# Kernel tuning notes

Measured on AMD Instinct MI355X. Metric: run time of the kernel, lower is better.

The kernel has to match this reference:

```python
import jax, jax.numpy as jnp
import numpy as np

# Hardware / quantization constants (DacAdcHardwareSettings + quant scales)
INPUT_BITS = 8
OUT_PREC_BITS = 8          # fractional precision bits of the ADC
OUT_RANGE_BITS = 4         # ADC full-scale range = 2**OUT_RANGE_BITS
VMAX = 0.6                 # DAC output voltage full scale
OUT_SCALE = 8020.0         # hardware_output_current_scaling (current -> ADC units)
INPUT_FACTOR = 0.15        # 1/(activation scale * quant_max)
OUTPUT_FACTOR = 0.01       # weight scale * activation scale * quant_max
G_SCALE = 1e-4             # conductance magnitude (Siemens) for memristor cells
WEIGHT_PRECISION = 4       # -> 3 bit-plane memristor arrays


def dac(x):
    # clamp to [-1,1], quantize to INPUT_BITS signed levels, scale to volts
    levels = 2.0 ** (INPUT_BITS - 1) - 1.0
    return VMAX * jnp.round(jnp.clip(x, -1.0, 1.0) * levels) / levels


def adc(current):
    # scale current to ADC units, quantize with fixed fractional step, clip to range
    step = 2.0 ** (-OUT_PREC_BITS)
    rng = 2.0 ** OUT_RANGE_BITS
    scaled = current * OUT_SCALE
    return jnp.clip(jnp.round(scaled / step) * step, -rng, rng)


def setup_inputs() -> dict:
    key = jax.random.key(0)
    k0, k1, k2, k3 = jax.random.split(key, 4)
    tokens, d_in, d_out = 8192, 4096, 4096
    n_planes = WEIGHT_PRECISION - 1
    x = jax.random.normal(k0, (tokens, d_in), dtype=jnp.float32)
    # paired memristor conductances per bit plane, input-major [plane, in, out]
    w_pos = jax.random.uniform(k1, (n_planes, d_in, d_out), dtype=jnp.float32) * G_SCALE
    w_neg = jax.random.uniform(k2, (n_planes, d_in, d_out), dtype=jnp.float32) * G_SCALE
    bias = jax.random.normal(k3, (d_out,), dtype=jnp.float32)
    return {"x": x, "w_pos": w_pos, "w_neg": w_neg, "bias": bias}


def reference(x, w_pos, w_neg, bias):
    # DAC: quantize scaled activations to drive voltages
    inp = dac(x * INPUT_FACTOR)                      # [B, I]
    # effective bit-plane weights: positive minus negative cell conductances
    w_eff = w_pos - w_neg                            # [P, I, O]
    # crossbar readout for all bit planes: I = V @ G
    planes = jnp.einsum('bi,pio->pbo', inp, w_eff)   # [P, B, O]
    q = adc(planes)                                  # quantized per plane
    # shift-accumulate: memristors[-1] is bit 0; memristors[i] (i<P-2) is bit P-2-i
    p = w_eff.shape[0]
    shifts = jnp.array([2.0 ** (p - 1 - i) for i in range(p)],
                       dtype=x.dtype)
    shifts = shifts.at[-1].set(1.0)                  # [4., 2., 1.] for precision 4
    mem_out = jnp.einsum('pbo,p->bo', q, shifts)
    return mem_out * OUTPUT_FACTOR + bias
```

## Files before the change

### kernel.cpp

```cpp
#include <hip/hip_runtime.h>
#include <hip/hip_bf16.h>
#include <stdint.h>

#define TOK  8192
#define DIN  4096
#define DOUT 4096
#define NPL  3

typedef unsigned short u16;
typedef __attribute__((ext_vector_type(8))) __bf16 bf16x8;
typedef __attribute__((ext_vector_type(4))) float f32x4;
typedef __attribute__((ext_vector_type(4))) unsigned short u16x4;

#define ADC_MUL   9699.7795275590551f
#define INV256    0.00390625f

#define GL(src, dst) __builtin_amdgcn_global_load_lds( \
    (const __attribute__((address_space(1))) void*)(src), \
    (__attribute__((address_space(3))) void*)(dst), 16, 0, 0)

__global__ void dac_kernel(const float* __restrict__ x, u16* __restrict__ a) {
    const int n4 = TOK * DIN / 4;
    int i = blockIdx.x * blockDim.x + threadIdx.x;
    const int stride = gridDim.x * blockDim.x;
    const float4* xv = (const float4*)x;
    u16x4* av = (u16x4*)a;
    for (; i < n4; i += stride) {
        float4 v = xv[i];
        u16x4 o;
        float t, k;
        t = v.x * 0.15f; t = fminf(1.0f, fmaxf(-1.0f, t)); k = rintf(t * 127.0f);
        o.x = (u16)(__float_as_uint(k) >> 16);
        t = v.y * 0.15f; t = fminf(1.0f, fmaxf(-1.0f, t)); k = rintf(t * 127.0f);
        o.y = (u16)(__float_as_uint(k) >> 16);
        t = v.z * 0.15f; t = fminf(1.0f, fmaxf(-1.0f, t)); k = rintf(t * 127.0f);
        o.z = (u16)(__float_as_uint(k) >> 16);
        t = v.w * 0.15f; t = fminf(1.0f, fmaxf(-1.0f, t)); k = rintf(t * 127.0f);
        o.w = (u16)(__float_as_uint(k) >> 16);
        av[i] = o;
    }
}

__global__ void wsplit_kernel(const float* __restrict__ wp, const float* __restrict__ wn,
                              u16* __restrict__ w) {
    __shared__ float tile[64][65];
    const int b   = blockIdx.x;
    const int p   = b >> 12;
    const int rem = b & 4095;
    const int ib  = rem >> 6, ob = rem & 63;
    const int t   = threadIdx.x;
    const size_t plane = (size_t)p * DIN * DOUT;

    {
        const int o4 = (t & 15) << 2;
        const int r0 = t >> 4;
#pragma unroll
        for (int pass = 0; pass < 4; ++pass) {
            const int r = (pass << 4) + r0;
            const size_t off = plane + (size_t)(ib * 64 + r) * DOUT + ob * 64 + o4;
            const float4 a = *(const float4*)(wp + off);
            const float4 c = *(const float4*)(wn + off);
            tile[r][o4 + 0] = a.x - c.x;
            tile[r][o4 + 1] = a.y - c.y;
            tile[r][o4 + 2] = a.z - c.z;
            tile[r][o4 + 3] = a.w - c.w;
        }
    }
    __syncthreads();
    const int lane = t & 63, w4 = t >> 6;
#pragma unroll
    for (int pass = 0; pass < 16; ++pass) {
        const int o = (pass << 2) + w4;
        float d = tile[lane][o];
        uint32_t db = __float_as_uint(d);
        uint32_t hb = (db + 0x7fffu + ((db >> 16) & 1u)) & 0xffff0000u;
        float l = d - __uint_as_float(hb);
        uint32_t lb = __float_as_uint(l);
        u16 lo16 = (u16)((lb + 0x7fffu + ((lb >> 16) & 1u)) >> 16);
        size_t base = (size_t)(ob * 64 + o) * 24576 + (size_t)p * 8192 + ib * 128 + lane;
        w[base]      = (u16)(hb >> 16);
        w[base + 64] = lo16;
    }
}

#define PHASE(AREG, BOFF, KOFF, STAGE_STMT, WAIT_STMT)                                  \
    {                                                                                   \
        bf16x8 bR[4];                                                                   \
        _Pragma("unroll")                                                               \
        for (int ni = 0; ni < 4; ++ni)                                                  \
            bR[ni] = *(const bf16x8*)(lB + (BOFF) + bRd + (ni << 11) + (KOFF));         \
        STAGE_STMT;                                                                     \
        __builtin_amdgcn_s_barrier();                                                   \
        asm volatile("s_waitcnt lgkmcnt(0)" ::: "memory");                              \
        __builtin_amdgcn_sched_barrier(0);                                              \
        __builtin_amdgcn_s_setprio(1);                                                  \
        _Pragma("unroll")                                                               \
        for (int mi = 0; mi < 4; ++mi)                                                  \
            _Pragma("unroll")                                                           \
            for (int ni = 0; ni < 4; ++ni)                                              \
                acc[mi][ni] = __builtin_amdgcn_mfma_f32_16x16x32_bf16(                  \
                    AREG[mi], bR[ni], acc[mi][ni], 0, 0, 0);                            \
        __builtin_amdgcn_s_setprio(0);                                                  \
        WAIT_STMT;                                                                      \
        __builtin_amdgcn_s_barrier();                                                   \
    }

__global__ __launch_bounds__(512, 2) void gemm_kernel(
    const u16* __restrict__ A,
    const u16* __restrict__ W,
    const float* __restrict__ bias,
    float* __restrict__ out)
{
    __shared__ __align__(16) char lds[131072];

    const int bid = blockIdx.x;
    const int g   = ((bid & 7) << 7) | (bid >> 3);
    const int mblk = g & 31, nblk = g >> 5;
    const int row0 = mblk << 8, col0 = nblk << 7;

    const int tid = threadIdx.x, lane = tid & 63, wid = tid >> 6;
    const int wm = wid >> 1, wn = wid & 1;

    const int swzb = (((tid & 7) ^ ((tid >> 3) & 7)) << 4);
    const char* gA = (const char*)A;
    const char* gB = (const char*)W;
    const size_t aRow = (size_t)(row0 + (tid >> 3)) * 8192 + swzb;
    const size_t bRow = (size_t)(col0 + (tid >> 3)) * 49152 + swzb;
    const int dstL = wid << 10;

    const int koff0 = (((lane >> 4) + 0) ^ (lane & 7)) << 4;
    const int koff1 = (((lane >> 4) + 4) ^ (lane & 7)) << 4;
    const int aRd = ((wm << 6) + (lane & 15)) << 7;
    const int bRd = ((wn << 6) + (lane & 15)) << 7;

    f32x4 acc[4][4], fin[4][4];
#pragma unroll
    for (int i = 0; i < 4; ++i)
#pragma unroll
        for (int j = 0; j < 4; ++j) {
            acc[i][j] = (f32x4){0.f, 0.f, 0.f, 0.f};
            fin[i][j] = (f32x4){0.f, 0.f, 0.f, 0.f};
        }

    auto stageA = [&](int it1, int j, char* dst) {
        GL(gA + aRow + ((size_t)j << 19) + ((size_t)(it1 & 63) << 7),
           dst + (j << 13) + dstL);
    };
    auto stageBhi = [&](int it1, int j, char* dst) {
        GL(gB + bRow + (size_t)it1 * 256 + ((size_t)j << 6) * 49152,
           dst + (j << 13) + dstL);
    };
    auto stageBlo = [&](int it1, int j, char* dst) {
        GL(gB + bRow + (size_t)it1 * 256 + 128 + ((size_t)j << 6) * 49152,
           dst + 16384 + (j << 13) + dstL);
    };

    {
        char* a0 = lds;
        char* b0 = lds + 65536;
        stageA(0, 0, a0); stageA(0, 1, a0); stageA(0, 2, a0); stageA(0, 3, a0);
        stageBhi(0, 0, b0); stageBhi(0, 1, b0);
        stageBlo(0, 0, b0); stageBlo(0, 1, b0);
        asm volatile("s_waitcnt vmcnt(2)" ::: "memory");
        __builtin_amdgcn_s_barrier();
    }

    for (int it = 0; it < 192; ++it) {
        const int buf = it & 1;
        const char* lA = lds + (buf << 15);
        const char* lB = lds + 65536 + (buf << 15);
        char* sA1 = lds + ((buf ^ 1) << 15);
        char* sB1 = lds + 65536 + ((buf ^ 1) << 15);
        const bool st = (it < 191);

        bf16x8 aR0[4], aR1[4];
#pragma unroll
        for (int mi = 0; mi < 4; ++mi)
            aR0[mi] = *(const bf16x8*)(lA + aRd + (mi << 11) + koff0);
#pragma unroll
        for (int mi = 0; mi < 4; ++mi)
            aR1[mi] = *(const bf16x8*)(lA + aRd + (mi << 11) + koff1);

        PHASE(aR0, 0, koff0,
              { if (st) { stageA(it + 1, 0, sA1); stageA(it + 1, 1, sA1); } }, {});
        PHASE(aR1, 0, koff1,
              { if (st) { stageA(it + 1, 2, sA1); stageA(it + 1, 3, sA1); } },
              { if (st) asm volatile("s_waitcnt vmcnt(4)" ::: "memory");
                else    asm volatile("s_waitcnt vmcnt(0)" ::: "memory"); });
        PHASE(aR0, 16384, koff0,
              { if (st) { stageBhi(it + 1, 0, sB1); stageBhi(it + 1, 1, sB1); } }, {});
        PHASE(aR1, 16384, koff1,
              { if (st) { stageBlo(it + 1, 0, sB1); stageBlo(it + 1, 1, sB1); } },
              { if (st) asm volatile("s_waitcnt vmcnt(2)" ::: "memory");
                else    asm volatile("s_waitcnt vmcnt(0)" ::: "memory"); });

        if ((it & 63) == 63) {
            const float sh = (it == 63) ? 4.f : (it == 127) ? 2.f : 1.f;
#pragma unroll
            for (int mi = 0; mi < 4; ++mi)
#pragma unroll
                for (int ni = 0; ni < 4; ++ni)
#pragma unroll
                    for (int r = 0; r < 4; ++r) {
                        float q = rintf(acc[mi][ni][r] * ADC_MUL) * INV256;
                        q = fminf(16.0f, fmaxf(-16.0f, q));
                        fin[mi][ni][r] += sh * q;
                        acc[mi][ni][r] = 0.f;
                    }
        }
    }

    const int orow0 = row0 + (wm << 6) + ((lane >> 4) << 2);
    const int ocol0 = col0 + (wn << 6) + (lane & 15);
#pragma unroll
    for (int ni = 0; ni < 4; ++ni) {
        const int c = ocol0 + (ni << 4);
        const float bv = bias[c];
#pragma unroll
        for (int mi = 0; mi < 4; ++mi)
#pragma unroll
            for (int r = 0; r < 4; ++r)
                out[(size_t)(orow0 + (mi << 4) + r) * DOUT + c] = fin[mi][ni][r] * 0.01f + bv;
    }
}

extern "C" void kernel_launch(void* const* d_in, const int* in_sizes, int n_in,
                              void* d_out, int out_size, void* d_ws, size_t ws_size,
                              hipStream_t stream) {
    const float* x    = (const float*)d_in[0];
    const float* wp   = (const float*)d_in[1];
    const float* wn   = (const float*)d_in[2];
    const float* bias = (const float*)d_in[3];
    float* out = (float*)d_out;

    u16* A = (u16*)d_ws;
    u16* W = A + (size_t)TOK * DIN;

    dac_kernel<<<dim3(4096), dim3(256), 0, stream>>>(x, A);
    wsplit_kernel<<<dim3(NPL * 64 * 64), dim3(256), 0, stream>>>(wp, wn, W);
    gemm_kernel<<<dim3(1024), dim3(512), 0, stream>>>(A, W, bias, out);
}
```

Before: 1.861 ms.

## Software-pipeline LDS fragment reads with MFMA and vectorize weight-prep stores

```diff
diff --git a/kernel.cpp b/kernel.cpp
--- a/kernel.cpp
+++ b/kernel.cpp
@@ -11,6 +11,7 @@
 typedef __attribute__((ext_vector_type(8))) __bf16 bf16x8;
 typedef __attribute__((ext_vector_type(4))) float f32x4;
 typedef __attribute__((ext_vector_type(4))) unsigned short u16x4;
+typedef __attribute__((ext_vector_type(8))) unsigned short u16x8;
 
 #define ADC_MUL   9699.7795275590551f
 #define INV256    0.00390625f
@@ -18,6 +19,11 @@
 #define GL(src, dst) __builtin_amdgcn_global_load_lds( \
     (const __attribute__((address_space(1))) void*)(src), \
     (__attribute__((address_space(3))) void*)(dst), 16, 0, 0)
+
+__device__ __forceinline__ u16 rne_bf16(float f) {
+    uint32_t b = __float_as_uint(f);
+    return (u16)((b + 0x7fffu + ((b >> 16) & 1u)) >> 16);
+}
 
 __global__ void dac_kernel(const float* __restrict__ x, u16* __restrict__ a) {
     const int n4 = TOK * DIN / 4;
@@ -60,50 +66,56 @@
             const size_t off = plane + (size_t)(ib * 64 + r) * DOUT + ob * 64 + o4;
             const float4 a = *(const float4*)(wp + off);
             const float4 c = *(const float4*)(wn + off);
-            tile[r][o4 + 0] = a.x - c.x;
-            tile[r][o4 + 1] = a.y - c.y;
-            tile[r][o4 + 2] = a.z - c.z;
-            tile[r][o4 + 3] = a.w - c.w;
+            tile[o4 + 0][r] = a.x - c.x;
+            tile[o4 + 1][r] = a.y - c.y;
+            tile[o4 + 2][r] = a.z - c.z;
+            tile[o4 + 3][r] = a.w - c.w;
         }
     }
     __syncthreads();
-    const int lane = t & 63, w4 = t >> 6;
-#pragma unroll
-    for (int pass = 0; pass < 16; ++pass) {
-        const int o = (pass << 2) + w4;
-        float d = tile[lane][o];
-        uint32_t db = __float_as_uint(d);
-        uint32_t hb = (db + 0x7fffu + ((db >> 16) & 1u)) & 0xffff0000u;
-        float l = d - __uint_as_float(hb);
-        uint32_t lb = __float_as_uint(l);
-        u16 lo16 = (u16)((lb + 0x7fffu + ((lb >> 16) & 1u)) >> 16);
-        size_t base = (size_t)(ob * 64 + o) * 24576 + (size_t)p * 8192 + ib * 128 + lane;
-        w[base]      = (u16)(hb >> 16);
-        w[base + 64] = lo16;
-    }
-}
-
-#define PHASE(AREG, BOFF, KOFF, STAGE_STMT, WAIT_STMT)                                  \
-    {                                                                                   \
-        bf16x8 bR[4];                                                                   \
+#pragma unroll
+    for (int pass = 0; pass < 4; ++pass) {
+        const int c    = (pass << 8) + t;
+        const int o    = c >> 4;
+        const int sub  = c & 15;
+        const int half = sub >> 3;
+        const int k8   = (sub & 7) << 3;
+        u16x8 ov;
+#pragma unroll
+        for (int j = 0; j < 8; ++j) {
+            float d = tile[o][k8 + j];
+            uint32_t db = __float_as_uint(d);
+            uint32_t hb = (db + 0x7fffu + ((db >> 16) & 1u)) & 0xffff0000u;
+            float l = d - __uint_as_float(hb);
+            u16 hi16 = (u16)(hb >> 16);
+            u16 lo16 = rne_bf16(l);
+            ov[j] = half ? lo16 : hi16;
+        }
+        const size_t idx = (size_t)(ob * 64 + o) * 24576 + (size_t)p * 8192
+                         + ib * 128 + half * 64 + k8;
+        *(u16x8*)(w + idx) = ov;
+    }
+}
+
+#define READ_A(dst, base, koff)                                                         \
+    _Pragma("unroll")                                                                   \
+    for (int mi = 0; mi < 4; ++mi)                                                      \
+        dst[mi] = *(const bf16x8*)((base) + aRd + (mi << 11) + (koff));
+#define READ_B(dst, base, boff, koff)                                                   \
+    _Pragma("unroll")                                                                   \
+    for (int ni = 0; ni < 4; ++ni)                                                      \
+        dst[ni] = *(const bf16x8*)((base) + (boff) + bRd + (ni << 11) + (koff));
+#define MFMA16(Aset, Bset)                                                              \
+    __builtin_amdgcn_s_setprio(1);                                                      \
+    _Pragma("unroll")                                                                   \
+    for (int mi = 0; mi < 4; ++mi)                                                      \
         _Pragma("unroll")                                                               \
         for (int ni = 0; ni < 4; ++ni)                                                  \
-            bR[ni] = *(const bf16x8*)(lB + (BOFF) + bRd + (ni << 11) + (KOFF));         \
-        STAGE_STMT;                                                                     \
-        __builtin_amdgcn_s_barrier();                                                   \
-        asm volatile("s_waitcnt lgkmcnt(0)" ::: "memory");                              \
-        __builtin_amdgcn_sched_barrier(0);                                              \
-        __builtin_amdgcn_s_setprio(1);                                                  \
-        _Pragma("unroll")                                                               \
-        for (int mi = 0; mi < 4; ++mi)                                                  \
-            _Pragma("unroll")                                                           \
-            for (int ni = 0; ni < 4; ++ni)                                              \
-                acc[mi][ni] = __builtin_amdgcn_mfma_f32_16x16x32_bf16(                  \
-                    AREG[mi], bR[ni], acc[mi][ni], 0, 0, 0);                            \
-        __builtin_amdgcn_s_setprio(0);                                                  \
-        WAIT_STMT;                                                                      \
-        __builtin_amdgcn_s_barrier();                                                   \
-    }
+            acc[mi][ni] = __builtin_amdgcn_mfma_f32_16x16x32_bf16(                      \
+                Aset[mi], Bset[ni], acc[mi][ni], 0, 0, 0);                              \
+    __builtin_amdgcn_s_setprio(0);
+#define SBAR  __builtin_amdgcn_sched_barrier(0)
+#define LGKM0 asm volatile("s_waitcnt lgkmcnt(0)" ::: "memory")
 
 __global__ __launch_bounds__(512, 2) void gemm_kernel(
     const u16* __restrict__ A,
@@ -155,6 +167,8 @@
            dst + 16384 + (j << 13) + dstL);
     };
 
+    bf16x8 fA0[4], fA1[4], fBa[4], fBb[4];
+
     {
         char* a0 = lds;
         char* b0 = lds + 65536;
@@ -163,36 +177,50 @@
         stageBlo(0, 0, b0); stageBlo(0, 1, b0);
         asm volatile("s_waitcnt vmcnt(2)" ::: "memory");
         __builtin_amdgcn_s_barrier();
+        READ_A(fA0, lds, koff0);
+        READ_B(fBa, lds + 65536, 0, koff0);
+        LGKM0;
     }
 
     for (int it = 0; it < 192; ++it) {
         const int buf = it & 1;
-        const char* lA = lds + (buf << 15);
-        const char* lB = lds + 65536 + (buf << 15);
-        char* sA1 = lds + ((buf ^ 1) << 15);
-        char* sB1 = lds + 65536 + ((buf ^ 1) << 15);
+        const char* lA  = lds + (buf << 15);
+        const char* lB  = lds + 65536 + (buf << 15);
+        char* sAn = lds + ((buf ^ 1) << 15);
+        char* sBn = lds + 65536 + ((buf ^ 1) << 15);
         const bool st = (it < 191);
 
-        bf16x8 aR0[4], aR1[4];
-#pragma unroll
-        for (int mi = 0; mi < 4; ++mi)
-            aR0[mi] = *(const bf16x8*)(lA + aRd + (mi << 11) + koff0);
-#pragma unroll
-        for (int mi = 0; mi < 4; ++mi)
-            aR1[mi] = *(const bf16x8*)(lA + aRd + (mi << 11) + koff1);
-
-        PHASE(aR0, 0, koff0,
-              { if (st) { stageA(it + 1, 0, sA1); stageA(it + 1, 1, sA1); } }, {});
-        PHASE(aR1, 0, koff1,
-              { if (st) { stageA(it + 1, 2, sA1); stageA(it + 1, 3, sA1); } },
-              { if (st) asm volatile("s_waitcnt vmcnt(4)" ::: "memory");
-                else    asm volatile("s_waitcnt vmcnt(0)" ::: "memory"); });
-        PHASE(aR0, 16384, koff0,
-              { if (st) { stageBhi(it + 1, 0, sB1); stageBhi(it + 1, 1, sB1); } }, {});
-        PHASE(aR1, 16384, koff1,
-              { if (st) { stageBlo(it + 1, 0, sB1); stageBlo(it + 1, 1, sB1); } },
-              { if (st) asm volatile("s_waitcnt vmcnt(2)" ::: "memory");
-                else    asm volatile("s_waitcnt vmcnt(0)" ::: "memory"); });
+        if (st) { stageA(it + 1, 0, sAn); stageA(it + 1, 1, sAn); }
+        READ_A(fA1, lA, koff1);
+        READ_B(fBb, lB, 0, koff1);
+        SBAR;
+        MFMA16(fA0, fBa);
+        SBAR; LGKM0;
+
+        if (st) { stageA(it + 1, 2, sAn); stageA(it + 1, 3, sAn); }
+        if (st) { asm volatile("s_waitcnt vmcnt(4)" ::: "memory"); }
+        else    { asm volatile("s_waitcnt vmcnt(0)" ::: "memory"); }
+        __builtin_amdgcn_s_barrier();
+        READ_B(fBa, lB, 16384, koff0);
+        SBAR;
+        MFMA16(fA1, fBb);
+        SBAR; LGKM0;
+
+        if (st) { stageBhi(it + 1, 0, sBn); stageBhi(it + 1, 1, sBn); }
+        READ_B(fBb, lB, 16384, koff1);
+        SBAR;
+        MFMA16(fA0, fBa);
+        SBAR; LGKM0;
+
+        if (st) { stageBlo(it + 1, 0, sBn); stageBlo(it + 1, 1, sBn); }
+        if (st) { asm volatile("s_waitcnt vmcnt(2)" ::: "memory"); }
+        else    { asm volatile("s_waitcnt vmcnt(0)" ::: "memory"); }
+        __builtin_amdgcn_s_barrier();
+        READ_A(fA0, sAn, koff0);
+        READ_B(fBa, sBn, 0, koff0);
+        SBAR;
+        MFMA16(fA1, fBb);
+        SBAR; LGKM0;
 
         if ((it & 63) == 63) {
             const float sh = (it == 63) ? 4.f : (it == 127) ? 2.f : 1.f;
```

Result: slower. 1.973 ms (+6.0%).
